# Kernel tuning notes

Measured on AMD Instinct MI355X. Metric: run time of the kernel, lower is better.

## Reference

```python
import jax, jax.numpy as jnp
import numpy as np

B_COEF = 0.1          # position-offset scale 'b'
STRIDE = (1, 1)
PADDING = (1, 1)


def setup_inputs() -> dict:
    key = jax.random.key(0)
    k1, k2, k3 = jax.random.split(key, 3)
    x = jax.random.normal(k1, (16, 64, 128, 128), dtype=jnp.float32)
    kernel = jax.random.normal(k2, (128, 64, 3, 3), dtype=jnp.float32)
    bias = jax.random.normal(k3, (128,), dtype=jnp.float32)
    return {"x": x, "kernel": kernel, "bias": bias}


def _conv(inp, w):
    pads = [(PADDING[0], PADDING[0]), (PADDING[1], PADDING[1])]
    return jax.lax.conv_general_dilated(
        inp, w, window_strides=STRIDE, padding=pads,
        dimension_numbers=("NCHW", "OIHW", "NCHW"))


def reference(x, kernel, bias):
    # out[b,o,p] = sum_i x_unf[b,i,p] * (kernel_flat[o,i] + b*grid[p]) + bias[o]
    # = conv(x, kernel) + b*grid[p] * sum_i x_unf[b,i,p] + bias  (rank-1 separable)
    kh, kw = kernel.shape[2], kernel.shape[3]
    main = _conv(x, kernel)                                  # (B, O, Ho, Wo)
    H_out, W_out = main.shape[2], main.shape[3]

    # sum over in_channels and kernel window = ones-conv of channel-summed input
    ones_k = jnp.ones((1, 1, kh, kw), dtype=x.dtype)
    patch_sum = _conv(x.sum(axis=1, keepdims=True), ones_k)  # (B, 1, Ho, Wo)

    # Replicate torch meshgrid(arange(W_out), arange(H_out), indexing='ij')
    # -> flatten (W,H) row-major -> consumed as (H,W) row-major by the view.
    gx = jnp.arange(W_out)[:, None] + jnp.arange(H_out)[None, :]  # (Wo, Ho)
    grid2d = gx.reshape(-1).reshape(H_out, W_out).astype(x.dtype)  # (Ho, Wo)

    return main + B_COEF * grid2d * patch_sum + bias[None, :, None, None]
```

## Files before the change

### kernel.cpp

```cpp
#include <hip/hip_runtime.h>
#include <hip/hip_bf16.h>


typedef __attribute__((ext_vector_type(8))) short short8;
typedef __attribute__((ext_vector_type(4))) float f32x4;

#define B_COEF 0.1f
constexpr int CI = 64, CO = 128, H = 128, W = 128;
constexpr int XPAD = 72;

static __device__ inline short bf16s(float v) {
    __hip_bfloat16 b = __float2bfloat16(v);
    return *reinterpret_cast<short*>(&b);
}

static __device__ inline void bar_lgkm() {
    asm volatile("s_waitcnt lgkmcnt(0)" ::: "memory");
    __builtin_amdgcn_s_barrier();
    asm volatile("" ::: "memory");
}


__global__ void prep_wq(const float* __restrict__ wgt, __hip_bfloat16* __restrict__ wq) {
    int idx = blockIdx.x * 256 + threadIdx.x;
    if (idx < 9 * CO * CI) {
        int tap = idx >> 13;
        int rem = idx & 8191;
        int oc = rem >> 6, ci = rem & 63;
        int kc = ci >> 5, j = ci & 31;
        wq[(((tap * 2 + kc) * CO + oc) << 5) + j] =
            __float2bfloat16(wgt[(oc * CI + ci) * 9 + tap]);
    }
}

__global__ __launch_bounds__(256, 3)
void conv_fused(const float* __restrict__ x,
                const __hip_bfloat16* __restrict__ wq,
                const float* __restrict__ bias,
                float* __restrict__ out) {
    __shared__ __hip_bfloat16 xrow[3][130 * 64];
    __shared__ float psum[256];
    __shared__ float ssumL[130];

    const int tid = threadIdx.x, bx = blockIdx.x, b = blockIdx.y;
    const int h = ((bx & 7) << 4) | (bx >> 3);
    const int lane = tid & 63, waveid = tid >> 6;
    const int lo16 = lane & 15, quad = lane >> 4;
    const int m0 = (waveid & 1) * 64, n0 = (waveid >> 1) * 64;

    short8 bq[2][2][4];
#pragma unroll
    for (int kc = 0; kc < 2; ++kc)
#pragma unroll
        for (int ni = 0; ni < 4; ++ni)
            bq[0][kc][ni] = *(const short8*)(
                wq + ((kc * CO + n0 + ni * 16 + lo16) << 5) + quad * 8);

    if (tid < 48) {
        const int r = tid >> 4, s = ((tid >> 3) & 1) ? 129 : 0, u = tid & 7;
        short8 z = {0, 0, 0, 0, 0, 0, 0, 0};
        *(short8*)&xrow[r][s * 64 + ((u ^ (s & 7)) * 8)] = z;
    }

    const int wl = tid & 127, cg0 = tid >> 7;
    const int wslot = wl + 1, wsw = wslot & 7;
    float sacc = 0.0f;
    const float* xb = x + (size_t)b * CI * H * W + wl;
#pragma unroll
    for (int p = 0; p < 4; ++p) {
        const int cg = cg0 + 2 * p;
#pragma unroll
        for (int r = 0; r < 3; ++r) {
            const int gh = h - 1 + r;
            short8 pk = {0, 0, 0, 0, 0, 0, 0, 0};
            if (gh >= 0 && gh < H) {
                const float* px = xb + ((size_t)(cg * 8) * H + gh) * W;
                float v[8];
#pragma unroll
                for (int j = 0; j < 8; ++j) v[j] = px[(size_t)j * H * W];
#pragma unroll
                for (int j = 0; j < 8; ++j) {
                    pk[j] = bf16s(v[j]);
                    sacc += v[j];
                }
            }
            *(short8*)&xrow[r][wslot * 64 + ((cg ^ wsw) * 8)] = pk;
        }
    }
    psum[tid] = sacc;
    bar_lgkm();

    if (tid < 128) ssumL[tid + 1] = psum[tid] + psum[tid + 128];
    if (tid == 128) ssumL[0] = 0.0f;
    if (tid == 129) ssumL[129] = 0.0f;
    bar_lgkm();

    f32x4 acc[4][4] = {};

    __builtin_amdgcn_s_setprio(1);
#pragma unroll
    for (int tap = 0; tap < 9; ++tap) {
        const int pp = tap & 1;
        if (tap < 8) {
            const int tn = tap + 1;
#pragma unroll
            for (int kc = 0; kc < 2; ++kc)
#pragma unroll
                for (int ni = 0; ni < 4; ++ni)
                    bq[pp ^ 1][kc][ni] = *(const short8*)(
                        wq + (((tn * 2 + kc) * CO + n0 + ni * 16 + lo16) << 5) + quad * 8);
        }
        const int kh = tap / 3, kw = tap - kh * 3;
        const __hip_bfloat16* xs = &xrow[kh][0];
#pragma unroll
        for (int kc = 0; kc < 2; ++kc) {
            short8 af[4];
#pragma unroll
            for (int mi = 0; mi < 4; ++mi) {
                const int row = m0 + mi * 16 + lo16 + kw;
                af[mi] = *(const short8*)
                    &xs[row * 64 + (((kc * 4 + quad) ^ (row & 7)) * 8)];
            }
#pragma unroll
            for (int mi = 0; mi < 4; ++mi)
#pragma unroll
                for (int ni = 0; ni < 4; ++ni)
                    acc[mi][ni] = __builtin_amdgcn_mfma_f32_16x16x32_bf16(
                        af[mi], bq[pp][kc][ni], acc[mi][ni], 0, 0, 0);
        }
    }
    __builtin_amdgcn_s_setprio(0);

#pragma unroll
    for (int mi = 0; mi < 4; ++mi) {
        const int wbase = m0 + mi * 16 + quad * 4;
        float cs[6];
#pragma unroll
        for (int t = 0; t < 6; ++t) cs[t] = ssumL[wbase + t];
        float ps[4], cf[4];
#pragma unroll
        for (int t = 0; t < 4; ++t) {
            ps[t] = cs[t] + cs[t + 1] + cs[t + 2];
            cf[t] = B_COEF * (float)(h + wbase + t);
        }
#pragma unroll
        for (int ni = 0; ni < 4; ++ni) {
            const int oc = n0 + ni * 16 + lo16;
            const float bv = bias[oc];
            f32x4 v = acc[mi][ni];
#pragma unroll
            for (int t = 0; t < 4; ++t) v[t] = v[t] + cf[t] * ps[t] + bv;
            *(f32x4*)(out + (((size_t)b * CO + oc) * H + h) * W + wbase) = v;
        }
    }
}


constexpr int WPAD = 72;

__global__ void prep_w_fb(const float* __restrict__ wgt, __hip_bfloat16* __restrict__ wt) {
    int idx = blockIdx.x * 256 + threadIdx.x;
    if (idx < 9 * CO * CI) {
        int tap = idx / (CO * CI);
        int rem = idx - tap * (CO * CI);
        int oc = rem >> 6, ci = rem & 63;
        wt[idx] = __float2bfloat16(wgt[(oc * CI + ci) * 9 + tap]);
    }
}

__global__ __launch_bounds__(256, 2)
void conv_fb(const float* __restrict__ x, const __hip_bfloat16* __restrict__ wt,
             const float* __restrict__ bias, float* __restrict__ out) {
    __shared__ __hip_bfloat16 xrow[130 * XPAD];
    __shared__ __hip_bfloat16 wlds[CO * WPAD];
    __shared__ float colsum[132];

    const int tid = threadIdx.x;
    const int h = blockIdx.x, b = blockIdx.y;
    const int lane = tid & 63, waveid = tid >> 6;
    const int lo16 = lane & 15, quad = lane >> 4;
    const int m0 = (waveid & 1) * 64, n0 = (waveid >> 1) * 64;

    f32x4 acc[4][4] = {};
    if (tid < 132) colsum[tid] = 0.0f;
    const float* xb = x + (size_t)b * CI * H * W;

    const int w16 = tid & 15, cipl = (tid >> 4) & 3, rest0 = tid >> 6;

    for (int kh = 0; kh < 3; ++kh) {
        const int gh = h - 1 + kh;
        __syncthreads();
        for (int it = 0; it < 18; ++it) {
            int rest = rest0 + it * 4;
            int whi = rest % 9, ciph = rest / 9;
            int w = whi * 16 + w16;
            int ci0 = (ciph * 4 + cipl) * 2;
            int gw = w - 1;
            float x0 = 0.0f, x1 = 0.0f;
            if (w < 130 && gw >= 0 && gw < W && gh >= 0 && gh < H) {
                const float* p = xb + (size_t)ci0 * (H * W) + gh * W + gw;
                x0 = p[0];
                x1 = p[H * W];
            }
            if (w < 130) {
                __hip_bfloat162 pk;
                pk.x = __float2bfloat16(x0);
                pk.y = __float2bfloat16(x1);
                *(__hip_bfloat162*)&xrow[w * XPAD + ci0] = pk;
            }
            float cs = x0 + x1;
            cs += __shfl_xor(cs, 16);
            cs += __shfl_xor(cs, 32);
            if (quad == 0 && w < 130) atomicAdd(&colsum[w], cs);
        }
        for (int kw = 0; kw < 3; ++kw) {
            __syncthreads();
            {
                const __hip_bfloat16* wtap = wt + (kh * 3 + kw) * (CO * CI);
#pragma unroll
                for (int it = 0; it < 4; ++it) {
                    int j = tid + it * 256;
                    int oc = j >> 3, ch = (j & 7) * 8;
                    short8 v = *(const short8*)(wtap + oc * CI + ch);
                    *(short8*)&wlds[oc * WPAD + ch] = v;
                }
            }
            __syncthreads();
#pragma unroll
            for (int kc = 0; kc < 2; ++kc) {
                const int krow = kc * 32 + quad * 8;
                short8 af[4], bf[4];
#pragma unroll
                for (int mi = 0; mi < 4; ++mi)
                    af[mi] = *(const short8*)&xrow[(m0 + mi * 16 + lo16 + kw) * XPAD + krow];
#pragma unroll
                for (int ni = 0; ni < 4; ++ni)
                    bf[ni] = *(const short8*)&wlds[(n0 + ni * 16 + lo16) * WPAD + krow];
#pragma unroll
                for (int mi = 0; mi < 4; ++mi)
#pragma unroll
                    for (int ni = 0; ni < 4; ++ni)
                        acc[mi][ni] = __builtin_amdgcn_mfma_f32_16x16x32_bf16(
                            af[mi], bf[ni], acc[mi][ni], 0, 0, 0);
            }
        }
    }
    __syncthreads();
#pragma unroll
    for (int mi = 0; mi < 4; ++mi) {
        const int wbase = m0 + mi * 16 + quad * 4;
        float cs[6];
#pragma unroll
        for (int r = 0; r < 6; ++r) cs[r] = colsum[wbase + r];
        float ps[4], cf[4];
#pragma unroll
        for (int r = 0; r < 4; ++r) {
            ps[r] = cs[r] + cs[r + 1] + cs[r + 2];
            cf[r] = B_COEF * (float)(h + wbase + r);
        }
#pragma unroll
        for (int ni = 0; ni < 4; ++ni) {
            const int oc = n0 + ni * 16 + lo16;
            const float bv = bias[oc];
            f32x4 v = acc[mi][ni];
#pragma unroll
            for (int r = 0; r < 4; ++r) v[r] = v[r] + cf[r] * ps[r] + bv;
            *(f32x4*)(out + (((size_t)b * CO + oc) * H + h) * W + wbase) = v;
        }
    }
}


extern "C" void kernel_launch(void* const* d_in, const int* in_sizes, int n_in,
                              void* d_out, int out_size, void* d_ws, size_t ws_size,
                              hipStream_t stream) {
    const float* x    = (const float*)d_in[0];
    const float* wgt  = (const float*)d_in[1];
    const float* bias = (const float*)d_in[2];
    float* out = (float*)d_out;

    const size_t WQ_BYTES = (size_t)9 * 2 * CO * 32 * 2;

    if (ws_size >= WQ_BYTES) {
        __hip_bfloat16* wq = (__hip_bfloat16*)d_ws;
        prep_wq<<<dim3(288), dim3(256), 0, stream>>>(wgt, wq);
        conv_fused<<<dim3(H, 16), dim3(256), 0, stream>>>(x, wq, bias, out);
    } else {
        __hip_bfloat16* wt = (__hip_bfloat16*)d_ws;
        prep_w_fb<<<dim3(288), dim3(256), 0, stream>>>(wgt, wt);
        conv_fb<<<dim3(H, 16), dim3(256), 0, stream>>>(x, wt, bias, out);
    }
}
```

Measured before the change: 225.5 us.

## Make conv kernel persistent over row tiles and double-buffer input loads

Turns the conv kernel into a persistent grid of 768 blocks that loop over the 2048 (batch, row) tiles with a stride of 768, rather than launching one block per tile. It also splits the input staging into 24-float register chunks so the next channel group's global loads are in flight while the current one is converted to bf16 and written to LDS. The intent is to cut block launch and tail overhead and improve memory-level parallelism during staging. The costs are uneven work per block (2048/768 is not an integer), an extra barrier per iteration, and higher register pressure under the 3-blocks-per-CU launch bound.

```diff
diff --git a/kernel.cpp b/kernel.cpp
--- a/kernel.cpp
+++ b/kernel.cpp
@@ -33,6 +33,38 @@
     }
 }
 
+static __device__ __forceinline__ void load24(const float* __restrict__ xb, int h,
+                                              int cg, float* __restrict__ buf) {
+#pragma unroll
+    for (int r = 0; r < 3; ++r) {
+        const int gh = h - 1 + r;
+        if ((unsigned)gh < (unsigned)H) {
+            const float* px = xb + ((size_t)(cg * 8) * H + gh) * W;
+#pragma unroll
+            for (int j = 0; j < 8; ++j) buf[r * 8 + j] = px[(size_t)j * H * W];
+        } else {
+#pragma unroll
+            for (int j = 0; j < 8; ++j) buf[r * 8 + j] = 0.0f;
+        }
+    }
+}
+
+static __device__ __forceinline__ void proc24(__hip_bfloat16 (*xrow)[130 * 64],
+                                              int wslot, int wsw, int cg,
+                                              const float* __restrict__ buf,
+                                              float& sacc) {
+#pragma unroll
+    for (int r = 0; r < 3; ++r) {
+        short8 pk;
+#pragma unroll
+        for (int j = 0; j < 8; ++j) {
+            pk[j] = bf16s(buf[r * 8 + j]);
+            sacc += buf[r * 8 + j];
+        }
+        *(short8*)&xrow[r][wslot * 64 + ((cg ^ wsw) * 8)] = pk;
+    }
+}
+
 __global__ __launch_bounds__(256, 3)
 void conv_fused(const float* __restrict__ x,
                 const __hip_bfloat16* __restrict__ wq,
@@ -42,115 +74,108 @@
     __shared__ float psum[256];
     __shared__ float ssumL[130];
 
-    const int tid = threadIdx.x, bx = blockIdx.x, b = blockIdx.y;
-    const int h = ((bx & 7) << 4) | (bx >> 3);
+    const int tid = threadIdx.x, bid = blockIdx.x;
     const int lane = tid & 63, waveid = tid >> 6;
     const int lo16 = lane & 15, quad = lane >> 4;
     const int m0 = (waveid & 1) * 64, n0 = (waveid >> 1) * 64;
-
-    short8 bq[2][2][4];
-#pragma unroll
-    for (int kc = 0; kc < 2; ++kc)
-#pragma unroll
-        for (int ni = 0; ni < 4; ++ni)
-            bq[0][kc][ni] = *(const short8*)(
-                wq + ((kc * CO + n0 + ni * 16 + lo16) << 5) + quad * 8);
+    const int wl = tid & 127, cg0 = tid >> 7;
+    const int wslot = wl + 1, wsw = wslot & 7;
 
     if (tid < 48) {
         const int r = tid >> 4, s = ((tid >> 3) & 1) ? 129 : 0, u = tid & 7;
         short8 z = {0, 0, 0, 0, 0, 0, 0, 0};
         *(short8*)&xrow[r][s * 64 + ((u ^ (s & 7)) * 8)] = z;
     }
-
-    const int wl = tid & 127, cg0 = tid >> 7;
-    const int wslot = wl + 1, wsw = wslot & 7;
-    float sacc = 0.0f;
-    const float* xb = x + (size_t)b * CI * H * W + wl;
-#pragma unroll
-    for (int p = 0; p < 4; ++p) {
-        const int cg = cg0 + 2 * p;
-#pragma unroll
-        for (int r = 0; r < 3; ++r) {
-            const int gh = h - 1 + r;
-            short8 pk = {0, 0, 0, 0, 0, 0, 0, 0};
-            if (gh >= 0 && gh < H) {
-                const float* px = xb + ((size_t)(cg * 8) * H + gh) * W;
-                float v[8];
-#pragma unroll
-                for (int j = 0; j < 8; ++j) v[j] = px[(size_t)j * H * W];
-#pragma unroll
-                for (int j = 0; j < 8; ++j) {
-                    pk[j] = bf16s(v[j]);
-                    sacc += v[j];
-                }
-            }
-            *(short8*)&xrow[r][wslot * 64 + ((cg ^ wsw) * 8)] = pk;
-        }
-    }
-    psum[tid] = sacc;
-    bar_lgkm();
-
-    if (tid < 128) ssumL[tid + 1] = psum[tid] + psum[tid + 128];
     if (tid == 128) ssumL[0] = 0.0f;
     if (tid == 129) ssumL[129] = 0.0f;
-    bar_lgkm();
-
-    f32x4 acc[4][4] = {};
-
-    __builtin_amdgcn_s_setprio(1);
-#pragma unroll
-    for (int tap = 0; tap < 9; ++tap) {
-        const int pp = tap & 1;
-        if (tap < 8) {
-            const int tn = tap + 1;
-#pragma unroll
-            for (int kc = 0; kc < 2; ++kc)
-#pragma unroll
-                for (int ni = 0; ni < 4; ++ni)
-                    bq[pp ^ 1][kc][ni] = *(const short8*)(
-                        wq + (((tn * 2 + kc) * CO + n0 + ni * 16 + lo16) << 5) + quad * 8);
-        }
-        const int kh = tap / 3, kw = tap - kh * 3;
-        const __hip_bfloat16* xs = &xrow[kh][0];
-#pragma unroll
-        for (int kc = 0; kc < 2; ++kc) {
-            short8 af[4];
-#pragma unroll
-            for (int mi = 0; mi < 4; ++mi) {
-                const int row = m0 + mi * 16 + lo16 + kw;
-                af[mi] = *(const short8*)
-                    &xs[row * 64 + (((kc * 4 + quad) ^ (row & 7)) * 8)];
-            }
-#pragma unroll
-            for (int mi = 0; mi < 4; ++mi)
-#pragma unroll
-                for (int ni = 0; ni < 4; ++ni)
-                    acc[mi][ni] = __builtin_amdgcn_mfma_f32_16x16x32_bf16(
-                        af[mi], bq[pp][kc][ni], acc[mi][ni], 0, 0, 0);
-        }
-    }
-    __builtin_amdgcn_s_setprio(0);
-
-#pragma unroll
-    for (int mi = 0; mi < 4; ++mi) {
-        const int wbase = m0 + mi * 16 + quad * 4;
-        float cs[6];
-#pragma unroll
-        for (int t = 0; t < 6; ++t) cs[t] = ssumL[wbase + t];
-        float ps[4], cf[4];
-#pragma unroll
-        for (int t = 0; t < 4; ++t) {
-            ps[t] = cs[t] + cs[t + 1] + cs[t + 2];
-            cf[t] = B_COEF * (float)(h + wbase + t);
-        }
-#pragma unroll
-        for (int ni = 0; ni < 4; ++ni) {
-            const int oc = n0 + ni * 16 + lo16;
-            const float bv = bias[oc];
-            f32x4 v = acc[mi][ni];
-#pragma unroll
-            for (int t = 0; t < 4; ++t) v[t] = v[t] + cf[t] * ps[t] + bv;
-            *(f32x4*)(out + (((size_t)b * CO + oc) * H + h) * W + wbase) = v;
+
+    for (int t = bid; t < 2048; t += 768) {
+        const int b = t >> 7, u = t & 127;
+        const int h = ((u & 7) << 4) | (u >> 3);
+        const float* xb = x + (size_t)b * CI * H * W + wl;
+
+        bar_lgkm();
+
+        short8 bq[2][2][4];
+#pragma unroll
+        for (int kc = 0; kc < 2; ++kc)
+#pragma unroll
+            for (int ni = 0; ni < 4; ++ni)
+                bq[0][kc][ni] = *(const short8*)(
+                    wq + ((kc * CO + n0 + ni * 16 + lo16) << 5) + quad * 8);
+
+        float va[24], vb[24], sacc = 0.0f;
+        load24(xb, h, cg0, va);
+        load24(xb, h, cg0 + 2, vb);
+        proc24(xrow, wslot, wsw, cg0, va, sacc);
+        load24(xb, h, cg0 + 4, va);
+        proc24(xrow, wslot, wsw, cg0 + 2, vb, sacc);
+        load24(xb, h, cg0 + 6, vb);
+        proc24(xrow, wslot, wsw, cg0 + 4, va, sacc);
+        proc24(xrow, wslot, wsw, cg0 + 6, vb, sacc);
+        psum[tid] = sacc;
+        bar_lgkm();
+
+        if (tid < 128) ssumL[tid + 1] = psum[tid] + psum[tid + 128];
+        bar_lgkm();
+
+        f32x4 acc[4][4] = {};
+
+        __builtin_amdgcn_s_setprio(1);
+#pragma unroll
+        for (int tap = 0; tap < 9; ++tap) {
+            const int pp = tap & 1;
+            if (tap < 8) {
+                const int tn = tap + 1;
+#pragma unroll
+                for (int kc = 0; kc < 2; ++kc)
+#pragma unroll
+                    for (int ni = 0; ni < 4; ++ni)
+                        bq[pp ^ 1][kc][ni] = *(const short8*)(
+                            wq + (((tn * 2 + kc) * CO + n0 + ni * 16 + lo16) << 5) + quad * 8);
+            }
+            const int kh = tap / 3, kw = tap - kh * 3;
+            const __hip_bfloat16* xs = &xrow[kh][0];
+#pragma unroll
+            for (int kc = 0; kc < 2; ++kc) {
+                short8 af[4];
+#pragma unroll
+                for (int mi = 0; mi < 4; ++mi) {
+                    const int row = m0 + mi * 16 + lo16 + kw;
+                    af[mi] = *(const short8*)
+                        &xs[row * 64 + (((kc * 4 + quad) ^ (row & 7)) * 8)];
+                }
+#pragma unroll
+                for (int mi = 0; mi < 4; ++mi)
+#pragma unroll
+                    for (int ni = 0; ni < 4; ++ni)
+                        acc[mi][ni] = __builtin_amdgcn_mfma_f32_16x16x32_bf16(
+                            af[mi], bq[pp][kc][ni], acc[mi][ni], 0, 0, 0);
+            }
+        }
+        __builtin_amdgcn_s_setprio(0);
+
+#pragma unroll
+        for (int mi = 0; mi < 4; ++mi) {
+            const int wbase = m0 + mi * 16 + quad * 4;
+            float cs[6];
+#pragma unroll
+            for (int q2 = 0; q2 < 6; ++q2) cs[q2] = ssumL[wbase + q2];
+            float ps[4], cf[4];
+#pragma unroll
+            for (int q2 = 0; q2 < 4; ++q2) {
+                ps[q2] = cs[q2] + cs[q2 + 1] + cs[q2 + 2];
+                cf[q2] = B_COEF * (float)(h + wbase + q2);
+            }
+#pragma unroll
+            for (int ni = 0; ni < 4; ++ni) {
+                const int oc = n0 + ni * 16 + lo16;
+                const float bv = bias[oc];
+                f32x4 v = acc[mi][ni];
+#pragma unroll
+                for (int q2 = 0; q2 < 4; ++q2) v[q2] = v[q2] + cf[q2] * ps[q2] + bv;
+                *(f32x4*)(out + (((size_t)b * CO + oc) * H + h) * W + wbase) = v;
+            }
         }
     }
 }
@@ -284,7 +309,7 @@
     if (ws_size >= WQ_BYTES) {
         __hip_bfloat16* wq = (__hip_bfloat16*)d_ws;
         prep_wq<<<dim3(288), dim3(256), 0, stream>>>(wgt, wq);
-        conv_fused<<<dim3(H, 16), dim3(256), 0, stream>>>(x, wq, bias, out);
+        conv_fused<<<dim3(768), dim3(256), 0, stream>>>(x, wq, bias, out);
     } else {
         __hip_bfloat16* wt = (__hip_bfloat16*)d_ws;
         prep_w_fb<<<dim3(288), dim3(256), 0, stream>>>(wgt, wt);
```

Result: slower. 301.3 us (+33.6%).
